# Kernel optimization log

Hardware: AMD Instinct MI355X
Metric: run time of the kernel (lower is better)

Reference implementation:

```python
import jax, jax.numpy as jnp
import numpy as np

N, F = 2048, 128
HEADS, OUT_DIM = 8, 8
ALPHA = 0.2  # tf.nn.leaky_relu default


def setup_inputs() -> dict:
    key = jax.random.key(0)
    k1, k2, k3, k4 = jax.random.split(key, 4)
    X = jax.random.normal(k1, (N, F), dtype=jnp.float32)
    A = jax.random.randint(k2, (N, N), 0, 2, dtype=jnp.int32)
    W = jax.random.normal(k3, (F, OUT_DIM * HEADS), dtype=jnp.float32) * (1.0 / np.sqrt(F))
    attn_kernel = jax.random.normal(k4, (2 * OUT_DIM, 1), dtype=jnp.float32) * 0.1
    return {"X": X, "A": A, "W": W, "attn_kernel": attn_kernel}


def reference(X, A, W, attn_kernel):
    # h: [N, heads, out_dim]
    h = (X @ W).reshape(N, HEADS, OUT_DIM)
    # tensordot(concat(h_i, h_j), a) == h_i @ a1 + h_j @ a2 (linear before leaky_relu),
    # so avoid materializing the [N,N,heads,2*out_dim] tile-concat tensor.
    a1 = attn_kernel[:OUT_DIM, 0]
    a2 = attn_kernel[OUT_DIM:, 0]
    s1 = jnp.einsum('nhd,d->nh', h, a1)  # [N, heads]
    s2 = jnp.einsum('nhd,d->nh', h, a2)  # [N, heads]
    e = jax.nn.leaky_relu(s1[:, None, :] + s2[None, :, :], ALPHA)  # [N, N, heads]
    mask = (A > 0).astype(e.dtype)[:, :, None]
    e = e * mask - 1e9 * (1.0 - mask)
    attention = jax.nn.softmax(e, axis=1)  # softmax over neighbor axis (axis=1), as in source
    # Faithful to source: einsum 'nij,njh->nih' contracts the HEAD axis
    # (attention [N,N,heads] with h [N,heads,out_dim]) -> [N, N, out_dim]
    h_prime = jnp.einsum('nij,njh->nih', attention, h)
    h_prime = h_prime.reshape(-1, OUT_DIM * HEADS)  # [N*N/heads, out_dim*heads]
    return jax.nn.leaky_relu(h_prime, ALPHA)
```

## Files before the change

kernel.cpp:

```cpp
#include <hip/hip_runtime.h>

#define NN      2048
#define FDIM    128
#define HEADS   8
#define ODIM    8
#define HID     64
#define ALPHA   0.2f

__device__ __forceinline__ float lrelu(float x) {
    return x > 0.f ? x : ALPHA * x;
}

__global__ __launch_bounds__(64) void gat_prep(
        const float* __restrict__ X,
        const float* __restrict__ W,
        const float* __restrict__ ak,
        float* __restrict__ H,
        float* __restrict__ S1,
        float* __restrict__ S2) {
    const int n = blockIdx.x;
    const int t = threadIdx.x;

    __shared__ float Xs[FDIM];
    __shared__ float hs[HID];

    Xs[t]      = X[(size_t)n * FDIM + t];
    Xs[t + 64] = X[(size_t)n * FDIM + 64 + t];
    __syncthreads();

    float acc = 0.f;
    #pragma unroll 8
    for (int k = 0; k < FDIM; ++k)
        acc = fmaf(Xs[k], W[k * HID + t], acc);

    H[(size_t)n * HID + t] = acc;
    hs[t] = acc;
    __syncthreads();

    if (t < 16) {
        const int head = t & 7;
        const float* a = ak + ((t < 8) ? 0 : ODIM);
        float s = 0.f;
        #pragma unroll
        for (int d = 0; d < ODIM; ++d)
            s = fmaf(hs[head * ODIM + d], a[d], s);
        if (t < 8) S1[n * HEADS + head] = s;
        else       S2[n * HEADS + head] = s;
    }
}

__global__ __launch_bounds__(256, 4) void gat_fused(
        const int*   __restrict__ A,
        const float* __restrict__ H,
        const float* __restrict__ S1,
        const float* __restrict__ S2,
        float* __restrict__ out) {
    const int i    = blockIdx.x;
    const int t    = threadIdx.x;
    const int wave = t >> 6;
    const int lane = t & 63;

    __shared__ int   As[NN];
    __shared__ float hhS[HID];
    __shared__ float redL[4 * HEADS];
    __shared__ float LFs[HEADS];

    const int4* Arow4 = (const int4*)(A + (size_t)i * NN);
    ((int4*)As)[t]       = Arow4[t];
    ((int4*)As)[t + 256] = Arow4[t + 256];

    if (t < HID)
        hhS[t] = H[(size_t)i * HID + t];

    float s1r[HEADS];
    #pragma unroll
    for (int h = 0; h < HEADS; ++h) s1r[h] = S1[i * HEADS + h];

    __syncthreads();

    float ls[HEADS];
    #pragma unroll
    for (int h = 0; h < HEADS; ++h) ls[h] = 0.f;

    #pragma unroll
    for (int jj = 0; jj < 8; ++jj) {
        const int j = t + jj * 256;
        const float4 s2a = *(const float4*)(S2 + j * HEADS);
        const float4 s2b = *(const float4*)(S2 + j * HEADS + 4);
        const bool msk = As[j] > 0;
        const float s2v[8] = {s2a.x, s2a.y, s2a.z, s2a.w,
                              s2b.x, s2b.y, s2b.z, s2b.w};
        #pragma unroll
        for (int h = 0; h < HEADS; ++h) {
            const float x = s1r[h] + s2v[h];
            ls[h] += msk ? __expf(lrelu(x)) : 0.f;
        }
    }

    #pragma unroll
    for (int h = 0; h < HEADS; ++h) {
        float v = ls[h];
        #pragma unroll
        for (int off = 32; off; off >>= 1)
            v += __shfl_xor(v, off);
        if (lane == 0) redL[wave * HEADS + h] = v;
    }
    __syncthreads();

    if (t < HEADS) {
        float v = 0.f;
        #pragma unroll
        for (int w = 0; w < 4; ++w)
            v += redL[w * HEADS + t];
        LFs[t] = v;
    }
    __syncthreads();

    float hh[HID];
    #pragma unroll
    for (int h = 0; h < HEADS; ++h) {
        const float inv = 1.0f / LFs[h];
        #pragma unroll
        for (int d = 0; d < ODIM; ++d)
            hh[h * ODIM + d] = hhS[h * ODIM + d] * inv;
    }

    #pragma unroll
    for (int jj = 0; jj < 8; ++jj) {
        const int j = t + jj * 256;
        const float4 s2a = *(const float4*)(S2 + j * HEADS);
        const float4 s2b = *(const float4*)(S2 + j * HEADS + 4);
        const bool msk = As[j] > 0;
        const float s2v[8] = {s2a.x, s2a.y, s2a.z, s2a.w,
                              s2b.x, s2b.y, s2b.z, s2b.w};

        float p[HEADS];
        #pragma unroll
        for (int h = 0; h < HEADS; ++h) {
            const float x = s1r[h] + s2v[h];
            p[h] = msk ? __expf(lrelu(x)) : 0.f;
        }

        float o[ODIM];
        #pragma unroll
        for (int d = 0; d < ODIM; ++d) o[d] = 0.f;
        #pragma unroll
        for (int h = 0; h < HEADS; ++h) {
            #pragma unroll
            for (int d = 0; d < ODIM; ++d)
                o[d] = fmaf(p[h], hh[h * ODIM + d], o[d]);
        }

        const size_t base = ((size_t)i * NN + j) * ODIM;
        float4 o0, o1;
        o0.x = lrelu(o[0]); o0.y = lrelu(o[1]);
        o0.z = lrelu(o[2]); o0.w = lrelu(o[3]);
        o1.x = lrelu(o[4]); o1.y = lrelu(o[5]);
        o1.z = lrelu(o[6]); o1.w = lrelu(o[7]);
        *(float4*)(out + base)     = o0;
        *(float4*)(out + base + 4) = o1;
    }
}

extern "C" void kernel_launch(void* const* d_in, const int* in_sizes, int n_in,
                              void* d_out, int out_size, void* d_ws, size_t ws_size,
                              hipStream_t stream) {
    const float* X  = (const float*)d_in[0];
    const int*   A  = (const int*)  d_in[1];
    const float* W  = (const float*)d_in[2];
    const float* ak = (const float*)d_in[3];
    float* out = (float*)d_out;

    float* H  = (float*)d_ws;
    float* S1 = H  + (size_t)NN * HID;
    float* S2 = S1 + (size_t)NN * HEADS;

    gat_prep <<<NN,  64, 0, stream>>>(X, W, ak, H, S1, S2);
    gat_fused<<<NN, 256, 0, stream>>>(A, H, S1, S2, out);
}
```

Measured before the change: 178.7 us.

## Cache softmax numerators in registers and widen blocks to 512 threads

The fused kernel now uses 512 threads per row, and each thread owns 4 consecutive columns. Each thread reads its A entries straight from global memory as one int4, so the shared-memory staging of the adjacency row goes away. The exp values from the first pass are kept in registers (p[4][8]), which removes the second recomputation of the exponentials and the reload of S2. Row-uniform values (S1 and the normalized h) are forced into scalar registers with readfirstlane to ease vector register pressure. The trade-off is a different store pattern: each thread now writes 4 contiguous rows of 32 bytes, and more live registers are needed per thread.

```diff
diff --git a/kernel.cpp b/kernel.cpp
--- a/kernel.cpp
+++ b/kernel.cpp
@@ -9,6 +9,10 @@
 
 __device__ __forceinline__ float lrelu(float x) {
     return x > 0.f ? x : ALPHA * x;
+}
+
+__device__ __forceinline__ float rfl(float x) {
+    return __int_as_float(__builtin_amdgcn_readfirstlane(__float_as_int(x)));
 }
 
 __global__ __launch_bounds__(64) void gat_prep(
@@ -49,7 +53,7 @@
     }
 }
 
-__global__ __launch_bounds__(256, 4) void gat_fused(
+__global__ __launch_bounds__(512, 4) void gat_fused(
         const int*   __restrict__ A,
         const float* __restrict__ H,
         const float* __restrict__ S1,
@@ -60,40 +64,40 @@
     const int wave = t >> 6;
     const int lane = t & 63;
 
-    __shared__ int   As[NN];
     __shared__ float hhS[HID];
-    __shared__ float redL[4 * HEADS];
+    __shared__ float redL[8 * HEADS];
     __shared__ float LFs[HEADS];
-
-    const int4* Arow4 = (const int4*)(A + (size_t)i * NN);
-    ((int4*)As)[t]       = Arow4[t];
-    ((int4*)As)[t + 256] = Arow4[t + 256];
 
     if (t < HID)
         hhS[t] = H[(size_t)i * HID + t];
 
     float s1r[HEADS];
     #pragma unroll
-    for (int h = 0; h < HEADS; ++h) s1r[h] = S1[i * HEADS + h];
+    for (int h = 0; h < HEADS; ++h)
+        s1r[h] = rfl(S1[i * HEADS + h]);
 
-    __syncthreads();
+    const int4 av = ((const int4*)(A + (size_t)i * NN))[t];
+    const int aj[4] = {av.x, av.y, av.z, av.w};
 
+    float p[4][HEADS];
     float ls[HEADS];
     #pragma unroll
     for (int h = 0; h < HEADS; ++h) ls[h] = 0.f;
 
     #pragma unroll
-    for (int jj = 0; jj < 8; ++jj) {
-        const int j = t + jj * 256;
-        const float4 s2a = *(const float4*)(S2 + j * HEADS);
-        const float4 s2b = *(const float4*)(S2 + j * HEADS + 4);
-        const bool msk = As[j] > 0;
-        const float s2v[8] = {s2a.x, s2a.y, s2a.z, s2a.w,
-                              s2b.x, s2b.y, s2b.z, s2b.w};
+    for (int e = 0; e < 4; ++e) {
+        const int j = 4 * t + e;
+        const float4 sa = *(const float4*)(S2 + j * HEADS);
+        const float4 sb = *(const float4*)(S2 + j * HEADS + 4);
+        const bool msk = aj[e] > 0;
+        const float s2v[8] = {sa.x, sa.y, sa.z, sa.w,
+                              sb.x, sb.y, sb.z, sb.w};
         #pragma unroll
         for (int h = 0; h < HEADS; ++h) {
-            const float x = s1r[h] + s2v[h];
-            ls[h] += msk ? __expf(lrelu(x)) : 0.f;
+            const float x  = s1r[h] + s2v[h];
+            const float pe = msk ? __expf(lrelu(x)) : 0.f;
+            p[e][h] = pe;
+            ls[h]  += pe;
         }
     }
 
@@ -110,36 +114,24 @@
     if (t < HEADS) {
         float v = 0.f;
         #pragma unroll
-        for (int w = 0; w < 4; ++w)
+        for (int w = 0; w < 8; ++w)
             v += redL[w * HEADS + t];
         LFs[t] = v;
     }
     __syncthreads();
 
-    float hh[HID];
+    float hh_s[HID];
     #pragma unroll
     for (int h = 0; h < HEADS; ++h) {
         const float inv = 1.0f / LFs[h];
         #pragma unroll
         for (int d = 0; d < ODIM; ++d)
-            hh[h * ODIM + d] = hhS[h * ODIM + d] * inv;
+            hh_s[h * ODIM + d] = rfl(hhS[h * ODIM + d] * inv);
     }
 
     #pragma unroll
-    for (int jj = 0; jj < 8; ++jj) {
-        const int j = t + jj * 256;
-        const float4 s2a = *(const float4*)(S2 + j * HEADS);
-        const float4 s2b = *(const float4*)(S2 + j * HEADS + 4);
-        const bool msk = As[j] > 0;
-        const float s2v[8] = {s2a.x, s2a.y, s2a.z, s2a.w,
-                              s2b.x, s2b.y, s2b.z, s2b.w};
-
-        float p[HEADS];
-        #pragma unroll
-        for (int h = 0; h < HEADS; ++h) {
-            const float x = s1r[h] + s2v[h];
-            p[h] = msk ? __expf(lrelu(x)) : 0.f;
-        }
+    for (int e = 0; e < 4; ++e) {
+        const int j = 4 * t + e;
 
         float o[ODIM];
         #pragma unroll
@@ -148,7 +140,7 @@
         for (int h = 0; h < HEADS; ++h) {
             #pragma unroll
             for (int d = 0; d < ODIM; ++d)
-                o[d] = fmaf(p[h], hh[h * ODIM + d], o[d]);
+                o[d] = fmaf(p[e][h], hh_s[h * ODIM + d], o[d]);
         }
 
         const size_t base = ((size_t)i * NN + j) * ODIM;
@@ -176,5 +168,5 @@
     float* S2 = S1 + (size_t)NN * HEADS;
 
     gat_prep <<<NN,  64, 0, stream>>>(X, W, ak, H, S1, S2);
-    gat_fused<<<NN, 256, 0, stream>>>(A, H, S1, S2, out);
+    gat_fused<<<NN, 512, 0, stream>>>(A, H, S1, S2, out);
 }
```

After: 218.7 us. +22.4%, slower.
